# Kernel optimization log

Measured on AMD Instinct MI355X. Metric: run time of the kernel, lower is better.

## Reference

```python
import jax, jax.numpy as jnp
import numpy as np

INPUT_SIZE = 256
HIDDEN = 512
OUTPUT = 128
NUM_LAYERS = 2
BATCH = 20  # hard-coded by init_hidden(20) in the original module
SEQ = 2048


def _uniform(key, shape, bound):
    return jax.random.uniform(key, shape, jnp.float32, -bound, bound)


def setup_inputs() -> dict:
    key = jax.random.key(0)
    ks = jax.random.split(key, 12)
    k = 1.0 / np.sqrt(HIDDEN)  # torch nn.RNN init: U(-1/sqrt(H), 1/sqrt(H))
    inp = {
        "x": jax.random.normal(ks[0], (BATCH, SEQ, INPUT_SIZE), jnp.float32),
        "h0": jnp.zeros((NUM_LAYERS, BATCH, HIDDEN), jnp.float32),
        "W_ih0": _uniform(ks[1], (HIDDEN, INPUT_SIZE), k),
        "W_hh0": _uniform(ks[2], (HIDDEN, HIDDEN), k),
        "b_ih0": _uniform(ks[3], (HIDDEN,), k),
        "b_hh0": _uniform(ks[4], (HIDDEN,), k),
        "W_ih1": _uniform(ks[5], (HIDDEN, HIDDEN), k),
        "W_hh1": _uniform(ks[6], (HIDDEN, HIDDEN), k),
        "b_ih1": _uniform(ks[7], (HIDDEN,), k),
        "b_hh1": _uniform(ks[8], (HIDDEN,), k),
        "W_fc": _uniform(ks[9], (OUTPUT, HIDDEN), 1.0 / np.sqrt(HIDDEN)),
        "b_fc": _uniform(ks[10], (OUTPUT,), 1.0 / np.sqrt(HIDDEN)),
    }
    return inp


def _rnn_layer(inp, h_init, W_ih, W_hh, b_ih, b_hh):
    # Precompute input projection for all timesteps: [B, T, H]
    pre = jnp.einsum('bti,hi->bth', inp, W_ih) + b_ih

    def step(h, p_t):
        h_new = jnp.tanh(p_t + h @ W_hh.T + b_hh)  # [B, H]
        return h_new, h_new

    _, hs = jax.lax.scan(step, h_init, jnp.swapaxes(pre, 0, 1))  # hs: [T, B, H]
    return jnp.swapaxes(hs, 0, 1)  # [B, T, H]


def reference(x, h0, W_ih0, W_hh0, b_ih0, b_hh0, W_ih1, W_hh1, b_ih1, b_hh1, W_fc, b_fc):
    # 2-layer tanh RNN (eval mode: inter-layer dropout inactive) + final Linear on last timestep
    out = _rnn_layer(x, h0[0], W_ih0, W_hh0, b_ih0, b_hh0)
    out = _rnn_layer(out, h0[1], W_ih1, W_hh1, b_ih1, b_hh1)
    return out[:, -1, :] @ W_fc.T + b_fc  # [B, OUTPUT]
```

## Files before the change

kernel.cpp:

```cpp
#include <hip/hip_runtime.h>

#define TSEQ 2048
#define NB   20
#define NIN  256
#define NH   512
#define NOUT 128

typedef unsigned int   u32;
typedef unsigned short u16;
typedef _Float16 f16x2 __attribute__((ext_vector_type(2)));

#define SM_W     0
#define SM_HX    131072
#define SM_INP   (131072 + 2048)
#define SMEM_BYTES (131072 + 2048 + 2048)

__device__ __forceinline__ u32 packh2(float a, float b) {
  f16x2 p; p.x = (_Float16)a; p.y = (_Float16)b;
  return __builtin_bit_cast(u32, p);
}

__device__ __forceinline__ float dot2(u32 w, u32 h, float acc) {
  return __builtin_amdgcn_fdot2(__builtin_bit_cast(f16x2, w),
                                __builtin_bit_cast(f16x2, h), acc, false);
}

__device__ __forceinline__ int acq(const int* p) {
  return __hip_atomic_load(p, __ATOMIC_ACQUIRE, __HIP_MEMORY_SCOPE_AGENT);
}
__device__ __forceinline__ void rel(int* p, int v) {
  __hip_atomic_store(p, v, __ATOMIC_RELEASE, __HIP_MEMORY_SCOPE_AGENT);
}
__device__ __forceinline__ void spin_until(const int* p, int need, int& seen) {
  while (seen < need) {
    seen = acq(p);
    if (seen < need) __builtin_amdgcn_s_sleep(1);
  }
}

__device__ __forceinline__ void lds_barrier() {
  asm volatile("s_waitcnt lgkmcnt(0)\n\ts_barrier" ::: "memory");
}

template<int CTRL>
__device__ __forceinline__ float dpp_add(float x) {
  int v = __builtin_amdgcn_update_dpp(0, __builtin_bit_cast(int, x), CTRL, 0xF, 0xF, true);
  return x + __builtin_bit_cast(float, v);
}

template<int CTRL>
__device__ __forceinline__ u32 dpp_mov_u32(u32 x) {
  return (u32)__builtin_amdgcn_update_dpp(0, (int)x, CTRL, 0xF, 0xF, true);
}

__device__ __forceinline__ float fast_tanh(float x) {
  float xc = fminf(fmaxf(x, -15.f), 15.f);
  float e = __builtin_amdgcn_exp2f(xc * 2.8853900817779268f);
  return (e - 1.f) * __builtin_amdgcn_rcpf(e + 1.f);
}

__device__ __forceinline__ int hx_gran_off(int g, int c) {
  int pg = (g ^ (g >> 2)) & 15;
  return 64 * pg + 16 * (c ^ (g & 3));
}

__global__ __launch_bounds__(512, 2) void rnn_persist(
    const float* __restrict__ x,    const float* __restrict__ h0,
    const float* __restrict__ Wih0, const float* __restrict__ Whh0,
    const float* __restrict__ bih0, const float* __restrict__ bhh0,
    const float* __restrict__ Wih1, const float* __restrict__ Whh1,
    const float* __restrict__ bih1, const float* __restrict__ bhh1,
    u16* __restrict__ pre0, u32* __restrict__ out0,
    u16* __restrict__ pre1, float* __restrict__ h1f,
    int* __restrict__ flags)
{
  extern __shared__ char smem[];
  const int tid = threadIdx.x;
  const int bid = blockIdx.x;

  if (bid < 40) {
    u32* inp = (u32*)(smem + SM_INP);
    const int b = bid >> 1, half = bid & 1, t0 = half * 1024;
    const int n = tid;
    u32 wr[128];
    const float4* W4 = (const float4*)(Wih0 + (size_t)n * NIN);
#pragma unroll
    for (int j = 0; j < 64; j++) {
      float4 w = W4[j];
      wr[2*j] = packh2(w.x, w.y); wr[2*j+1] = packh2(w.z, w.w);
    }
    const float bias = bih0[n];
    const float* xb = x + ((size_t)b * TSEQ + t0) * NIN;
    u16* op = pre0 + ((size_t)b * TSEQ + t0) * NH;

    float2 r = make_float2(0.f, 0.f);
    if (tid < 128) r = ((const float2*)xb)[tid];
    int cur = 0;
    for (int t = 0; t < 1024; t++) {
      if (tid < 128) inp[cur * 256 + tid] = packh2(r.x, r.y);
      __syncthreads();
      if (t + 1 < 1024 && tid < 128)
        r = ((const float2*)(xb + (size_t)(t + 1) * NIN))[tid];
      float a0 = bias, a1 = 0.f;
      const uint4* xp = (const uint4*)(inp + cur * 256);
#pragma unroll
      for (int j = 0; j < 32; j++) {
        uint4 hv = xp[j];
        a0 = dot2(wr[4*j+0], hv.x, a0); a1 = dot2(wr[4*j+1], hv.y, a1);
        a0 = dot2(wr[4*j+2], hv.z, a0); a1 = dot2(wr[4*j+3], hv.w, a1);
      }
      op[((size_t)(t >> 3) * NH + n) * 8 + (t & 7)] =
          __builtin_bit_cast(u16, (_Float16)(a0 + a1));
      cur ^= 1;
      if (((t + 1) & 7) == 0) {
        __syncthreads();
        if (tid == 0) rel(flags + bid * 32, t + 1);
      }
    }
    return;
  }

  if (bid >= 60 && bid < 140) {
    uint2* WL  = (uint2*)(smem + SM_W);
    u32*   inp = (u32*)(smem + SM_INP);
    const int b = (bid - 60) >> 2, sub = (bid - 60) & 3;
    const int n = tid;
    u32 wr[192];
    const float4* W4 = (const float4*)(Wih1 + (size_t)n * NH);
#pragma unroll
    for (int j = 0; j < 96; j++) {
      float4 w = W4[j];
      wr[2*j] = packh2(w.x, w.y); wr[2*j+1] = packh2(w.z, w.w);
    }
#pragma unroll
    for (int j2 = 0; j2 < 32; j2++) {
      float4 w = W4[96 + j2];
      WL[j2 * NH + n] = make_uint2(packh2(w.x, w.y), packh2(w.z, w.w));
    }
    const float bias = bih1[n];
    __syncthreads();

    const u32* ip = out0 + (size_t)b * TSEQ * 256;
    u16* op = pre1 + (size_t)b * TSEQ * NH;
    const int* flagOut0 = flags + (40 + b) * 32;
    int* flagMy = flags + (60 + b * 4 + sub) * 32;
    int seen = 0, cur = 0;
#pragma unroll 1
    for (int c = sub; c < TSEQ / 8; c += 4) {
      const int tbase = c * 8;
      spin_until(flagOut0, tbase + 8, seen);
      u32 rin = (tid < 256) ? ip[(size_t)tbase * 256 + tid] : 0;
#pragma unroll 1
      for (int qq = 0; qq < 8; qq++) {
        const int t = tbase + qq;
        if (tid < 256) inp[cur * 256 + tid] = rin;
        __syncthreads();
        if (qq + 1 < 8 && tid < 256) rin = ip[(size_t)(t + 1) * 256 + tid];
        float a0 = bias, a1 = 0.f;
        const uint4* hp4 = (const uint4*)(inp + cur * 256);
#pragma unroll
        for (int j = 0; j < 48; j++) {
          uint4 hv = hp4[j];
          a0 = dot2(wr[4*j+0], hv.x, a0); a1 = dot2(wr[4*j+1], hv.y, a1);
          a0 = dot2(wr[4*j+2], hv.z, a0); a1 = dot2(wr[4*j+3], hv.w, a1);
        }
#pragma unroll
        for (int jj = 0; jj < 16; jj++) {
          uint4 hv = hp4[48 + jj];
          uint2 w0 = WL[(2*jj)   * NH + n];
          uint2 w1 = WL[(2*jj+1) * NH + n];
          a0 = dot2(w0.x, hv.x, a0); a1 = dot2(w0.y, hv.y, a1);
          a0 = dot2(w1.x, hv.z, a0); a1 = dot2(w1.y, hv.w, a1);
        }
        op[((size_t)(t >> 3) * NH + n) * 8 + (t & 7)] =
            __builtin_bit_cast(u16, (_Float16)(a0 + a1));
        cur ^= 1;
      }
      __syncthreads();
      if (tid == 0) rel(flagMy, tbase + 8);
    }
    return;
  }

  const bool isL0 = (bid < 60);
  const int b = isL0 ? (bid - 40) : (bid - 140);
  const float* Wg = isL0 ? Whh0 : Whh1;
  const float* bp = isL0 ? bhh0 : bhh1;

  uint4* WLw4 = (uint4*)(smem + SM_W);
  char*  hxc  = smem + SM_HX;

  const int lam = tid & 15;
  const int ns  = tid >> 4;

  u32 wj[12][16];
#pragma unroll
  for (int g = 0; g < 4; g++) {
#pragma unroll
    for (int m = 0; m < 3; m++) {
      const float4* Wr = (const float4*)(Wg + (size_t)(16 * ns + 4 * g + m) * NH + 32 * lam);
#pragma unroll
      for (int k4 = 0; k4 < 8; k4++) {
        float4 w = Wr[k4];
        wj[3*g+m][2*k4] = packh2(w.x, w.y); wj[3*g+m][2*k4+1] = packh2(w.z, w.w);
      }
    }
  }
#pragma unroll
  for (int g = 0; g < 4; g++) {
    const float4* Wr = (const float4*)(Wg + (size_t)(16 * ns + 4 * g + 3) * NH + 32 * lam);
#pragma unroll
    for (int q = 0; q < 4; q++) {
      float4 wA = Wr[2*q], wB = Wr[2*q+1];
      WLw4[(4 * g + q) * 512 + tid] =
          make_uint4(packh2(wA.x, wA.y), packh2(wA.z, wA.w),
                     packh2(wB.x, wB.y), packh2(wB.z, wB.w));
    }
  }
  const float bias = bp[tid];

  int hadr[4];
#pragma unroll
  for (int c = 0; c < 4; c++) hadr[c] = hx_gran_off(lam, c);
  const int wg = (tid >> 5) & 15, wc = (tid >> 3) & 3;
  const int waddr = hx_gran_off(wg, wc) + (tid & 7) * 2;
  const bool b0 = (tid & 1), b1 = (tid & 2), b2 = (tid & 4), b3 = (tid & 8);

  *(u16*)(hxc + waddr) =
      __builtin_bit_cast(u16, (_Float16)h0[((isL0 ? 0 : 1) * NB + b) * NH + tid]);
  __syncthreads();

  const uint4* pin4 =
      (const uint4*)((isL0 ? pre0 : pre1) + (size_t)b * TSEQ * NH);
  u32* o0p = out0 + (size_t)b * TSEQ * 256;
  int* flagOut0 = flags + (40 + b) * 32;
  const int* f0 = flags + (b * 2 + 0) * 32;
  const int* f1 = flags + (b * 2 + 1) * 32;
  const int* fpA = flags + (60 + b * 4 + 0) * 32;
  const int* fpB = flags + (60 + b * 4 + 1) * 32;
  const int* fpC = flags + (60 + b * 4 + 2) * 32;
  const int* fpD = flags + (60 + b * 4 + 3) * 32;
  int s0 = 0, s1 = 0, sA = 0, sB = 0, sC = 0, sD = 0;

  if (isL0) { spin_until(f0, 8, s0); }  else { spin_until(fpA, 8, sA); }
  uint4 pcur4 = pin4[tid];
  if (isL0) { spin_until(f0, 16, s0); } else { spin_until(fpB, 16, sB); }
  uint4 pnext4 = pin4[512 + tid];

#define ROW16(acc, WR)                                              \
    acc = dot2(WR[0],  hv0.x, acc); acc = dot2(WR[1],  hv0.y, acc); \
    acc = dot2(WR[2],  hv0.z, acc); acc = dot2(WR[3],  hv0.w, acc); \
    acc = dot2(WR[4],  hv1.x, acc); acc = dot2(WR[5],  hv1.y, acc); \
    acc = dot2(WR[6],  hv1.z, acc); acc = dot2(WR[7],  hv1.w, acc); \
    acc = dot2(WR[8],  hv2.x, acc); acc = dot2(WR[9],  hv2.y, acc); \
    acc = dot2(WR[10], hv2.z, acc); acc = dot2(WR[11], hv2.w, acc); \
    acc = dot2(WR[12], hv3.x, acc); acc = dot2(WR[13], hv3.y, acc); \
    acc = dot2(WR[14], hv3.z, acc); acc = dot2(WR[15], hv3.w, acc)

#define GROUP(gi, OUT)                                               \
  {                                                                  \
    const uint4 wvA = WLw4[(4*gi + 0) * 512 + tid];                  \
    const uint4 wvB = WLw4[(4*gi + 1) * 512 + tid];                  \
    float a0 = 0.f, a1 = 0.f, a2 = 0.f, a3 = 0.f;                    \
    ROW16(a0, wj[3*gi+0]);                                           \
    a3 = dot2(wvA.x, hv0.x, a3); a3 = dot2(wvA.y, hv0.y, a3);        \
    a3 = dot2(wvA.z, hv0.z, a3); a3 = dot2(wvA.w, hv0.w, a3);        \
    const uint4 wvC = WLw4[(4*gi + 2) * 512 + tid];                  \
    const uint4 wvD = WLw4[(4*gi + 3) * 512 + tid];                  \
    ROW16(a1, wj[3*gi+1]);                                           \
    a3 = dot2(wvB.x, hv1.x, a3); a3 = dot2(wvB.y, hv1.y, a3);        \
    a3 = dot2(wvB.z, hv1.z, a3); a3 = dot2(wvB.w, hv1.w, a3);        \
    ROW16(a2, wj[3*gi+2]);                                           \
    a3 = dot2(wvC.x, hv2.x, a3); a3 = dot2(wvC.y, hv2.y, a3);        \
    a3 = dot2(wvC.z, hv2.z, a3); a3 = dot2(wvC.w, hv2.w, a3);        \
    a3 = dot2(wvD.x, hv3.x, a3); a3 = dot2(wvD.y, hv3.y, a3);        \
    a3 = dot2(wvD.z, hv3.z, a3); a3 = dot2(wvD.w, hv3.w, a3);        \
    float t0 = dpp_add<0xB1>(a0), t1 = dpp_add<0xB1>(a1);            \
    float t2 = dpp_add<0xB1>(a2), t3 = dpp_add<0xB1>(a3);            \
    float u0 = b0 ? t1 : t0, u1 = b0 ? t3 : t2;                      \
    u0 = dpp_add<0x4E>(u0); u1 = dpp_add<0x4E>(u1);                  \
    OUT = b1 ? u1 : u0;                                              \
  }

  float hlast = 0.f;
#pragma unroll 1
  for (int c = 0; c < TSEQ / 8; c++) {
#pragma unroll 1
    for (int q = 0; q < 8; q++) {
      const int t = c * 8 + q;
      const int rbase = (t & 1) << 10;
      const int wbase = rbase ^ 1024;

      const uint4 hv0 = *(const uint4*)(hxc + rbase + hadr[0]);
      const uint4 hv1 = *(const uint4*)(hxc + rbase + hadr[1]);
      const uint4 hv2 = *(const uint4*)(hxc + rbase + hadr[2]);
      const uint4 hv3 = *(const uint4*)(hxc + rbase + hadr[3]);

      float G0, G1, G2, G3;
      GROUP(0, G0); GROUP(1, G1); GROUP(2, G2); GROUP(3, G3);
      G0 = dpp_add<0x124>(G0); G1 = dpp_add<0x124>(G1);
      G2 = dpp_add<0x124>(G2); G3 = dpp_add<0x124>(G3);
      float r0 = b2 ? G1 : G0, r1 = b2 ? G3 : G2;
      r0 = dpp_add<0x128>(r0); r1 = dpp_add<0x128>(r1);
      const float red = b3 ? r1 : r0;

      const u32 wlo  = (q & 4) ? pcur4.z : pcur4.x;
      const u32 whi  = (q & 4) ? pcur4.w : pcur4.y;
      const u32 wsel = (q & 2) ? whi : wlo;
      const u16 pq   = (u16)((q & 1) ? (wsel >> 16) : (wsel & 0xffffu));

      const float h = fast_tanh(red + bias + (float)__builtin_bit_cast(_Float16, pq));
      hlast = h;
      const u16 h16 = __builtin_bit_cast(u16, (_Float16)h);
      *(u16*)(hxc + wbase + waddr) = h16;

      if (isL0) {
        u32 v = (u32)h16;
        u32 nb = dpp_mov_u32<0xB1>(v);
        if (!(tid & 1)) o0p[(size_t)t * 256 + (tid >> 1)] = v | (nb << 16);
      }

      if (q == 7) __syncthreads();
      else        lds_barrier();
    }

    if (isL0 && tid == 0) rel(flagOut0, c * 8 + 8);

    pcur4 = pnext4;
    if (c < TSEQ / 8 - 2) {
      const int c2 = c + 2;
      const int need = 8 * (c2 + 1);
      if (isL0) {
        if (c2 < 128) { spin_until(f0, need, s0); }
        else          { spin_until(f1, need - 1024, s1); }
      } else {
        const int w = c2 & 3;
        if      (w == 0) { spin_until(fpA, need, sA); }
        else if (w == 1) { spin_until(fpB, need, sB); }
        else if (w == 2) { spin_until(fpC, need, sC); }
        else             { spin_until(fpD, need, sD); }
      }
      pnext4 = pin4[(size_t)c2 * 512 + tid];
    }
  }
#undef GROUP
#undef ROW16

  if (!isL0) h1f[(size_t)b * NH + tid] = hlast;
}

__global__ void fc_kernel(const float* __restrict__ h1f, const float* __restrict__ Wfc,
                          const float* __restrict__ bfc, float* __restrict__ out) {
  const int b = blockIdx.x, o = threadIdx.x;
  __shared__ float hs[NH];
  for (int i = o; i < NH; i += NOUT) hs[i] = h1f[(size_t)b * NH + i];
  __syncthreads();
  const float4* w4 = (const float4*)(Wfc + (size_t)o * NH);
  const float4* h4 = (const float4*)hs;
  float acc = bfc[o];
#pragma unroll 8
  for (int j = 0; j < NH / 4; j++) {
    float4 w = w4[j], h = h4[j];
    acc += w.x * h.x + w.y * h.y + w.z * h.z + w.w * h.w;
  }
  out[(size_t)b * NOUT + o] = acc;
}

extern "C" void kernel_launch(void* const* d_in, const int* in_sizes, int n_in,
                              void* d_out, int out_size, void* d_ws, size_t ws_size,
                              hipStream_t stream) {
  const float* x    = (const float*)d_in[0];
  const float* h0   = (const float*)d_in[1];
  const float* Wih0 = (const float*)d_in[2];
  const float* Whh0 = (const float*)d_in[3];
  const float* bih0 = (const float*)d_in[4];
  const float* bhh0 = (const float*)d_in[5];
  const float* Wih1 = (const float*)d_in[6];
  const float* Whh1 = (const float*)d_in[7];
  const float* bih1 = (const float*)d_in[8];
  const float* bhh1 = (const float*)d_in[9];
  const float* Wfc  = (const float*)d_in[10];
  const float* bfc  = (const float*)d_in[11];
  float* out = (float*)d_out;

  char* ws = (char*)d_ws;
  size_t off = 0;
  u16* pre0 = (u16*)(ws + off); off += (size_t)NB * TSEQ * NH * 2;
  u32* out0 = (u32*)(ws + off); off += (size_t)NB * TSEQ * (NH / 2) * 4;
  u16* pre1 = (u16*)(ws + off); off += (size_t)NB * TSEQ * NH * 2;
  float* h1f = (float*)(ws + off); off += (size_t)NB * NH * 4;
  int* flags = (int*)(ws + off);
  const size_t flagbytes = 160 * 32 * sizeof(int);

  hipMemsetAsync(flags, 0, flagbytes, stream);
  hipFuncSetAttribute((const void*)rnn_persist,
                      hipFuncAttributeMaxDynamicSharedMemorySize, SMEM_BYTES);
  rnn_persist<<<160, 512, SMEM_BYTES, stream>>>(
      x, h0, Wih0, Whh0, bih0, bhh0, Wih1, Whh1, bih1, bhh1,
      pre0, out0, pre1, h1f, flags);
  fc_kernel<<<NB, NOUT, 0, stream>>>(h1f, Wfc, bfc, out);
}
```

Baseline: 3.636 ms.

## Split each recurrent chain across two blocks with global-memory hidden-state exchange

Each batch element's recurrence per layer is now split across two workgroups, each owning half of the output rows (256), with its W_hh half fully held in registers. The LDS-resident weight portion goes away. Every timestep the two halves swap their new hidden halves through global memory using sc0 sc1 cache-bypassing loads and stores plus a per-step flag spin. This halves the dot-product work per step, but adds a cross-CU global round-trip and polling on the serial critical path of every timestep. Layer-1 input blocks now wait on two layer-0 producer flags, and the grid grows to 200 blocks.

```diff
diff --git a/kernel.cpp b/kernel.cpp
--- a/kernel.cpp
+++ b/kernel.cpp
@@ -15,6 +15,9 @@
 #define SM_INP   (131072 + 2048)
 #define SMEM_BYTES (131072 + 2048 + 2048)
 
+#define XFL_BASE 200
+#define FLAG_LINES 320
+
 __device__ __forceinline__ u32 packh2(float a, float b) {
   f16x2 p; p.x = (_Float16)a; p.y = (_Float16)b;
   return __builtin_bit_cast(u32, p);
@@ -38,8 +41,23 @@
   }
 }
 
-__device__ __forceinline__ void lds_barrier() {
-  asm volatile("s_waitcnt lgkmcnt(0)\n\ts_barrier" ::: "memory");
+__device__ __forceinline__ u32 ld_sc01(const u32* p) {
+  u32 v;
+  asm volatile("global_load_dword %0, %1, off sc0 sc1\n\ts_waitcnt vmcnt(0)"
+               : "=v"(v) : "v"(p) : "memory");
+  return v;
+}
+__device__ __forceinline__ void st_sc01(u32* p, u32 v) {
+  asm volatile("global_store_dword %0, %1, off sc0 sc1" :: "v"(p), "v"(v) : "memory");
+}
+__device__ __forceinline__ void ld4x_sc01(const u32* p, uint4& a, uint4& b,
+                                          uint4& c, uint4& d) {
+  asm volatile("global_load_dwordx4 %0, %4, off sc0 sc1\n\t"
+               "global_load_dwordx4 %1, %4, off offset:16 sc0 sc1\n\t"
+               "global_load_dwordx4 %2, %4, off offset:32 sc0 sc1\n\t"
+               "global_load_dwordx4 %3, %4, off offset:48 sc0 sc1\n\t"
+               "s_waitcnt vmcnt(0)"
+               : "=&v"(a), "=&v"(b), "=&v"(c), "=&v"(d) : "v"(p) : "memory");
 }
 
 template<int CTRL>
@@ -47,7 +65,6 @@
   int v = __builtin_amdgcn_update_dpp(0, __builtin_bit_cast(int, x), CTRL, 0xF, 0xF, true);
   return x + __builtin_bit_cast(float, v);
 }
-
 template<int CTRL>
 __device__ __forceinline__ u32 dpp_mov_u32(u32 x) {
   return (u32)__builtin_amdgcn_update_dpp(0, (int)x, CTRL, 0xF, 0xF, true);
@@ -62,6 +79,10 @@
 __device__ __forceinline__ int hx_gran_off(int g, int c) {
   int pg = (g ^ (g >> 2)) & 15;
   return 64 * pg + 16 * (c ^ (g & 3));
+}
+
+__device__ __forceinline__ uint4 sel4(bool c, uint4 a, uint4 b) {
+  return make_uint4(c ? a.x : b.x, c ? a.y : b.y, c ? a.z : b.z, c ? a.w : b.w);
 }
 
 __global__ __launch_bounds__(512, 2) void rnn_persist(
@@ -72,7 +93,7 @@
     const float* __restrict__ bih1, const float* __restrict__ bhh1,
     u16* __restrict__ pre0, u32* __restrict__ out0,
     u16* __restrict__ pre1, float* __restrict__ h1f,
-    int* __restrict__ flags)
+    int* __restrict__ flags, u32* __restrict__ xb)
 {
   extern __shared__ char smem[];
   const int tid = threadIdx.x;
@@ -90,17 +111,17 @@
       wr[2*j] = packh2(w.x, w.y); wr[2*j+1] = packh2(w.z, w.w);
     }
     const float bias = bih0[n];
-    const float* xb = x + ((size_t)b * TSEQ + t0) * NIN;
+    const float* xbp = x + ((size_t)b * TSEQ + t0) * NIN;
     u16* op = pre0 + ((size_t)b * TSEQ + t0) * NH;
 
     float2 r = make_float2(0.f, 0.f);
-    if (tid < 128) r = ((const float2*)xb)[tid];
+    if (tid < 128) r = ((const float2*)xbp)[tid];
     int cur = 0;
     for (int t = 0; t < 1024; t++) {
       if (tid < 128) inp[cur * 256 + tid] = packh2(r.x, r.y);
       __syncthreads();
       if (t + 1 < 1024 && tid < 128)
-        r = ((const float2*)(xb + (size_t)(t + 1) * NIN))[tid];
+        r = ((const float2*)(xbp + (size_t)(t + 1) * NIN))[tid];
       float a0 = bias, a1 = 0.f;
       const uint4* xp = (const uint4*)(inp + cur * 256);
 #pragma unroll
@@ -120,10 +141,10 @@
     return;
   }
 
-  if (bid >= 60 && bid < 140) {
+  if (bid >= 80 && bid < 160) {
     uint2* WL  = (uint2*)(smem + SM_W);
     u32*   inp = (u32*)(smem + SM_INP);
-    const int b = (bid - 60) >> 2, sub = (bid - 60) & 3;
+    const int b = (bid - 80) >> 2, sub = (bid - 80) & 3;
     const int n = tid;
     u32 wr[192];
     const float4* W4 = (const float4*)(Wih1 + (size_t)n * NH);
@@ -142,13 +163,15 @@
 
     const u32* ip = out0 + (size_t)b * TSEQ * 256;
     u16* op = pre1 + (size_t)b * TSEQ * NH;
-    const int* flagOut0 = flags + (40 + b) * 32;
-    int* flagMy = flags + (60 + b * 4 + sub) * 32;
-    int seen = 0, cur = 0;
+    const int* fH0 = flags + (40 + b * 2 + 0) * 32;
+    const int* fH1 = flags + (40 + b * 2 + 1) * 32;
+    int* flagMy = flags + (80 + b * 4 + sub) * 32;
+    int sH0 = 0, sH1 = 0, cur = 0;
 #pragma unroll 1
     for (int c = sub; c < TSEQ / 8; c += 4) {
       const int tbase = c * 8;
-      spin_until(flagOut0, tbase + 8, seen);
+      spin_until(fH0, tbase + 8, sH0);
+      spin_until(fH1, tbase + 8, sH1);
       u32 rin = (tid < 256) ? ip[(size_t)tbase * 256 + tid] : 0;
 #pragma unroll 1
       for (int qq = 0; qq < 8; qq++) {
@@ -182,105 +205,71 @@
     return;
   }
 
-  const bool isL0 = (bid < 60);
-  const int b = isL0 ? (bid - 40) : (bid - 140);
+  const bool isL0 = (bid < 160);
+  const int idx = isL0 ? (bid - 40) : (bid - 160);
+  const int b = idx >> 1, H = idx & 1, L = isL0 ? 0 : 1;
   const float* Wg = isL0 ? Whh0 : Whh1;
   const float* bp = isL0 ? bhh0 : bhh1;
 
-  uint4* WLw4 = (uint4*)(smem + SM_W);
-  char*  hxc  = smem + SM_HX;
+  char* hxc = smem + SM_HX;
 
   const int lam = tid & 15;
   const int ns  = tid >> 4;
-
-  u32 wj[12][16];
-#pragma unroll
-  for (int g = 0; g < 4; g++) {
-#pragma unroll
-    for (int m = 0; m < 3; m++) {
-      const float4* Wr = (const float4*)(Wg + (size_t)(16 * ns + 4 * g + m) * NH + 32 * lam);
-#pragma unroll
-      for (int k4 = 0; k4 < 8; k4++) {
-        float4 w = Wr[k4];
-        wj[3*g+m][2*k4] = packh2(w.x, w.y); wj[3*g+m][2*k4+1] = packh2(w.z, w.w);
-      }
-    }
-  }
-#pragma unroll
-  for (int g = 0; g < 4; g++) {
-    const float4* Wr = (const float4*)(Wg + (size_t)(16 * ns + 4 * g + 3) * NH + 32 * lam);
-#pragma unroll
-    for (int q = 0; q < 4; q++) {
-      float4 wA = Wr[2*q], wB = Wr[2*q+1];
-      WLw4[(4 * g + q) * 512 + tid] =
-          make_uint4(packh2(wA.x, wA.y), packh2(wA.z, wA.w),
-                     packh2(wB.x, wB.y), packh2(wB.z, wB.w));
-    }
-  }
-  const float bias = bp[tid];
+  const int rbase0 = 256 * H + 8 * ns;
+  const int n = rbase0 + (lam & 7);
+  const bool inhalf = H ? (lam >= 8) : (lam < 8);
+
+  u32 wj[8][16];
+#pragma unroll
+  for (int j = 0; j < 8; j++) {
+    const float4* Wr = (const float4*)(Wg + (size_t)(rbase0 + j) * NH + 32 * lam);
+#pragma unroll
+    for (int k4 = 0; k4 < 8; k4++) {
+      float4 w = Wr[k4];
+      wj[j][2*k4] = packh2(w.x, w.y); wj[j][2*k4+1] = packh2(w.z, w.w);
+    }
+  }
+  const float bias = bp[n];
 
   int hadr[4];
 #pragma unroll
   for (int c = 0; c < 4; c++) hadr[c] = hx_gran_off(lam, c);
-  const int wg = (tid >> 5) & 15, wc = (tid >> 3) & 3;
-  const int waddr = hx_gran_off(wg, wc) + (tid & 7) * 2;
-  const bool b0 = (tid & 1), b1 = (tid & 2), b2 = (tid & 4), b3 = (tid & 8);
-
-  *(u16*)(hxc + waddr) =
-      __builtin_bit_cast(u16, (_Float16)h0[((isL0 ? 0 : 1) * NB + b) * NH + tid]);
+  const int wgi = (n >> 5) & 15, wci = (n >> 3) & 3;
+  const int waddr = hx_gran_off(wgi, wci) + (n & 7) * 2;
+  const bool b0 = (tid & 1), b1 = (tid & 2), b2 = (tid & 4);
+
+  {
+    const int wg0 = (tid >> 5) & 15, wc0 = (tid >> 3) & 3;
+    *(u16*)(hxc + hx_gran_off(wg0, wc0) + (tid & 7) * 2) =
+        __builtin_bit_cast(u16, (_Float16)h0[(L * NB + b) * NH + tid]);
+  }
   __syncthreads();
 
-  const uint4* pin4 =
-      (const uint4*)((isL0 ? pre0 : pre1) + (size_t)b * TSEQ * NH);
+  u32* xb_my = xb + ((size_t)((L * 20 + b) * 2 + H) * 2) * 128;
+  const u32* xb_pt = xb + ((size_t)((L * 20 + b) * 2 + (1 - H)) * 2) * 128;
+  u32* xfl_my = (u32*)(flags + (XFL_BASE + (L * 20 + b) * 2 + H) * 32);
+  const u32* xfl_pt = (const u32*)(flags + (XFL_BASE + (L * 20 + b) * 2 + (1 - H)) * 32);
+  const int xoff = (16 * lam) & 127;
+
+  const uint4* pin4 = (const uint4*)((isL0 ? pre0 : pre1) + (size_t)b * TSEQ * NH);
   u32* o0p = out0 + (size_t)b * TSEQ * 256;
-  int* flagOut0 = flags + (40 + b) * 32;
+  int* flagOutH = flags + (40 + b * 2 + H) * 32;
   const int* f0 = flags + (b * 2 + 0) * 32;
   const int* f1 = flags + (b * 2 + 1) * 32;
-  const int* fpA = flags + (60 + b * 4 + 0) * 32;
-  const int* fpB = flags + (60 + b * 4 + 1) * 32;
-  const int* fpC = flags + (60 + b * 4 + 2) * 32;
-  const int* fpD = flags + (60 + b * 4 + 3) * 32;
+  const int* fpA = flags + (80 + b * 4 + 0) * 32;
+  const int* fpB = flags + (80 + b * 4 + 1) * 32;
+  const int* fpC = flags + (80 + b * 4 + 2) * 32;
+  const int* fpD = flags + (80 + b * 4 + 3) * 32;
   int s0 = 0, s1 = 0, sA = 0, sB = 0, sC = 0, sD = 0;
 
   if (isL0) { spin_until(f0, 8, s0); }  else { spin_until(fpA, 8, sA); }
-  uint4 pcur4 = pin4[tid];
+  uint4 pcur4 = pin4[n];
   if (isL0) { spin_until(f0, 16, s0); } else { spin_until(fpB, 16, sB); }
-  uint4 pnext4 = pin4[512 + tid];
-
-#define ROW16(acc, WR)                                              \
-    acc = dot2(WR[0],  hv0.x, acc); acc = dot2(WR[1],  hv0.y, acc); \
-    acc = dot2(WR[2],  hv0.z, acc); acc = dot2(WR[3],  hv0.w, acc); \
-    acc = dot2(WR[4],  hv1.x, acc); acc = dot2(WR[5],  hv1.y, acc); \
-    acc = dot2(WR[6],  hv1.z, acc); acc = dot2(WR[7],  hv1.w, acc); \
-    acc = dot2(WR[8],  hv2.x, acc); acc = dot2(WR[9],  hv2.y, acc); \
-    acc = dot2(WR[10], hv2.z, acc); acc = dot2(WR[11], hv2.w, acc); \
-    acc = dot2(WR[12], hv3.x, acc); acc = dot2(WR[13], hv3.y, acc); \
-    acc = dot2(WR[14], hv3.z, acc); acc = dot2(WR[15], hv3.w, acc)
-
-#define GROUP(gi, OUT)                                               \
-  {                                                                  \
-    const uint4 wvA = WLw4[(4*gi + 0) * 512 + tid];                  \
-    const uint4 wvB = WLw4[(4*gi + 1) * 512 + tid];                  \
-    float a0 = 0.f, a1 = 0.f, a2 = 0.f, a3 = 0.f;                    \
-    ROW16(a0, wj[3*gi+0]);                                           \
-    a3 = dot2(wvA.x, hv0.x, a3); a3 = dot2(wvA.y, hv0.y, a3);        \
-    a3 = dot2(wvA.z, hv0.z, a3); a3 = dot2(wvA.w, hv0.w, a3);        \
-    const uint4 wvC = WLw4[(4*gi + 2) * 512 + tid];                  \
-    const uint4 wvD = WLw4[(4*gi + 3) * 512 + tid];                  \
-    ROW16(a1, wj[3*gi+1]);                                           \
-    a3 = dot2(wvB.x, hv1.x, a3); a3 = dot2(wvB.y, hv1.y, a3);        \
-    a3 = dot2(wvB.z, hv1.z, a3); a3 = dot2(wvB.w, hv1.w, a3);        \
-    ROW16(a2, wj[3*gi+2]);                                           \
-    a3 = dot2(wvC.x, hv2.x, a3); a3 = dot2(wvC.y, hv2.y, a3);        \
-    a3 = dot2(wvC.z, hv2.z, a3); a3 = dot2(wvC.w, hv2.w, a3);        \
-    a3 = dot2(wvD.x, hv3.x, a3); a3 = dot2(wvD.y, hv3.y, a3);        \
-    a3 = dot2(wvD.z, hv3.z, a3); a3 = dot2(wvD.w, hv3.w, a3);        \
-    float t0 = dpp_add<0xB1>(a0), t1 = dpp_add<0xB1>(a1);            \
-    float t2 = dpp_add<0xB1>(a2), t3 = dpp_add<0xB1>(a3);            \
-    float u0 = b0 ? t1 : t0, u1 = b0 ? t3 : t2;                      \
-    u0 = dpp_add<0x4E>(u0); u1 = dpp_add<0x4E>(u1);                  \
-    OUT = b1 ? u1 : u0;                                              \
-  }
+  uint4 pnext4 = pin4[512 + n];
+
+  const bool pk_act = inhalf && !(lam & 1);
+  const int gidx = n >> 1;
+  const int lidx = gidx & 127;
 
   float hlast = 0.f;
 #pragma unroll 1
@@ -289,20 +278,50 @@
     for (int q = 0; q < 8; q++) {
       const int t = c * 8 + q;
       const int rbase = (t & 1) << 10;
-      const int wbase = rbase ^ 1024;
-
-      const uint4 hv0 = *(const uint4*)(hxc + rbase + hadr[0]);
-      const uint4 hv1 = *(const uint4*)(hxc + rbase + hadr[1]);
-      const uint4 hv2 = *(const uint4*)(hxc + rbase + hadr[2]);
-      const uint4 hv3 = *(const uint4*)(hxc + rbase + hadr[3]);
-
-      float G0, G1, G2, G3;
-      GROUP(0, G0); GROUP(1, G1); GROUP(2, G2); GROUP(3, G3);
+
+      uint4 g0 = make_uint4(0,0,0,0), g1 = g0, g2 = g0, g3 = g0;
+      if (t != 0) {
+        while (ld_sc01(xfl_pt) < (u32)t) __builtin_amdgcn_s_sleep(1);
+        ld4x_sc01(xb_pt + (size_t)((t - 1) & 1) * 128 + xoff, g0, g1, g2, g3);
+      }
+      const uint4 l0 = *(const uint4*)(hxc + rbase + hadr[0]);
+      const uint4 l1 = *(const uint4*)(hxc + rbase + hadr[1]);
+      const uint4 l2 = *(const uint4*)(hxc + rbase + hadr[2]);
+      const uint4 l3 = *(const uint4*)(hxc + rbase + hadr[3]);
+      const bool useL = inhalf || (t == 0);
+      const uint4 hv0 = sel4(useL, l0, g0);
+      const uint4 hv1 = sel4(useL, l1, g1);
+      const uint4 hv2 = sel4(useL, l2, g2);
+      const uint4 hv3 = sel4(useL, l3, g3);
+
+      float a0=0.f,a1=0.f,a2=0.f,a3=0.f,a4=0.f,a5=0.f,a6=0.f,a7=0.f;
+#define ROWD(acc, WR)                                               \
+      acc = dot2(WR[0],  hv0.x, acc); acc = dot2(WR[1],  hv0.y, acc); \
+      acc = dot2(WR[2],  hv0.z, acc); acc = dot2(WR[3],  hv0.w, acc); \
+      acc = dot2(WR[4],  hv1.x, acc); acc = dot2(WR[5],  hv1.y, acc); \
+      acc = dot2(WR[6],  hv1.z, acc); acc = dot2(WR[7],  hv1.w, acc); \
+      acc = dot2(WR[8],  hv2.x, acc); acc = dot2(WR[9],  hv2.y, acc); \
+      acc = dot2(WR[10], hv2.z, acc); acc = dot2(WR[11], hv2.w, acc); \
+      acc = dot2(WR[12], hv3.x, acc); acc = dot2(WR[13], hv3.y, acc); \
+      acc = dot2(WR[14], hv3.z, acc); acc = dot2(WR[15], hv3.w, acc)
+      ROWD(a0, wj[0]); ROWD(a1, wj[1]); ROWD(a2, wj[2]); ROWD(a3, wj[3]);
+      ROWD(a4, wj[4]); ROWD(a5, wj[5]); ROWD(a6, wj[6]); ROWD(a7, wj[7]);
+#undef ROWD
+
+      float t0 = dpp_add<0xB1>(a0), t1 = dpp_add<0xB1>(a1);
+      float t2 = dpp_add<0xB1>(a2), t3 = dpp_add<0xB1>(a3);
+      float u0 = b0 ? t1 : t0, u1 = b0 ? t3 : t2;
+      u0 = dpp_add<0x4E>(u0); u1 = dpp_add<0x4E>(u1);
+      float G0 = b1 ? u1 : u0;
+      t0 = dpp_add<0xB1>(a4); t1 = dpp_add<0xB1>(a5);
+      t2 = dpp_add<0xB1>(a6); t3 = dpp_add<0xB1>(a7);
+      u0 = b0 ? t1 : t0; u1 = b0 ? t3 : t2;
+      u0 = dpp_add<0x4E>(u0); u1 = dpp_add<0x4E>(u1);
+      float G1 = b1 ? u1 : u0;
       G0 = dpp_add<0x124>(G0); G1 = dpp_add<0x124>(G1);
-      G2 = dpp_add<0x124>(G2); G3 = dpp_add<0x124>(G3);
-      float r0 = b2 ? G1 : G0, r1 = b2 ? G3 : G2;
-      r0 = dpp_add<0x128>(r0); r1 = dpp_add<0x128>(r1);
-      const float red = b3 ? r1 : r0;
+      float r = b2 ? G1 : G0;
+      r = dpp_add<0x128>(r);
+      const float red = r;
 
       const u32 wlo  = (q & 4) ? pcur4.z : pcur4.x;
       const u32 whi  = (q & 4) ? pcur4.w : pcur4.y;
@@ -312,19 +331,25 @@
       const float h = fast_tanh(red + bias + (float)__builtin_bit_cast(_Float16, pq));
       hlast = h;
       const u16 h16 = __builtin_bit_cast(u16, (_Float16)h);
-      *(u16*)(hxc + wbase + waddr) = h16;
-
-      if (isL0) {
+      const int wbase = rbase ^ 1024;
+      if (inhalf) *(u16*)(hxc + wbase + waddr) = h16;
+
+      {
         u32 v = (u32)h16;
         u32 nb = dpp_mov_u32<0xB1>(v);
-        if (!(tid & 1)) o0p[(size_t)t * 256 + (tid >> 1)] = v | (nb << 16);
-      }
-
-      if (q == 7) __syncthreads();
-      else        lds_barrier();
-    }
-
-    if (isL0 && tid == 0) rel(flagOut0, c * 8 + 8);
+        u32 pk = v | (nb << 16);
+        if (pk_act) {
+          st_sc01(xb_my + (size_t)(t & 1) * 128 + lidx, pk);
+          if (isL0) o0p[(size_t)t * 256 + gidx] = pk;
+        }
+      }
+
+      asm volatile("s_waitcnt vmcnt(0) lgkmcnt(0)" ::: "memory");
+      __builtin_amdgcn_s_barrier();
+      if (tid == 0) st_sc01(xfl_my, (u32)(t + 1));
+    }
+
+    if (isL0 && tid == 0) rel(flagOutH, c * 8 + 8);
 
     pcur4 = pnext4;
     if (c < TSEQ / 8 - 2) {
@@ -340,13 +365,11 @@
         else if (w == 2) { spin_until(fpC, need, sC); }
         else             { spin_until(fpD, need, sD); }
       }
-      pnext4 = pin4[(size_t)c2 * 512 + tid];
-    }
-  }
-#undef GROUP
-#undef ROW16
-
-  if (!isL0) h1f[(size_t)b * NH + tid] = hlast;
+      pnext4 = pin4[(size_t)c2 * 512 + n];
+    }
+  }
+
+  if (!isL0 && inhalf) h1f[(size_t)b * NH + n] = hlast;
 }
 
 __global__ void fc_kernel(const float* __restrict__ h1f, const float* __restrict__ Wfc,
@@ -390,13 +413,15 @@
   u16* pre1 = (u16*)(ws + off); off += (size_t)NB * TSEQ * NH * 2;
   float* h1f = (float*)(ws + off); off += (size_t)NB * NH * 4;
   int* flags = (int*)(ws + off);
-  const size_t flagbytes = 160 * 32 * sizeof(int);
-
-  hipMemsetAsync(flags, 0, flagbytes, stream);
-  hipFuncSetAttribute((const void*)rnn_persist,
-                      hipFuncAttributeMaxDynamicSharedMemorySize, SMEM_BYTES);
-  rnn_persist<<<160, 512, SMEM_BYTES, stream>>>(
+  const size_t flagbytes = FLAG_LINES * 32 * sizeof(int);
+  off += flagbytes;
+  u32* xb = (u32*)(ws + off);
+
+  (void)hipMemsetAsync(flags, 0, flagbytes, stream);
+  (void)hipFuncSetAttribute((const void*)rnn_persist,
+                            hipFuncAttributeMaxDynamicSharedMemorySize, SMEM_BYTES);
+  rnn_persist<<<200, 512, SMEM_BYTES, stream>>>(
       x, h0, Wih0, Whh0, bih0, bhh0, Wih1, Whh1, bih1, bhh1,
-      pre0, out0, pre1, h1f, flags);
+      pre0, out0, pre1, h1f, flags, xb);
   fc_kernel<<<NB, NOUT, 0, stream>>>(h1f, Wfc, bfc, out);
 }
```

Result: slower. 7.415 ms (+103.9%).
